# Performance work log

Hardware: AMD Instinct MI355X
Metric: run time of the kernel (lower is better)

## Reference

```python
import jax, jax.numpy as jnp
import numpy as np

B, N, D = 32, 2048, 256


def setup_inputs() -> dict:
    key = jax.random.key(0)
    ks = jax.random.split(key, 9)
    s = 1.0 / np.sqrt(D)
    return {
        "x": jax.random.normal(ks[0], (B, N, D), dtype=jnp.float32),
        "Wq": jax.random.normal(ks[1], (D, D), dtype=jnp.float32) * s,
        "bq": jax.random.normal(ks[2], (D,), dtype=jnp.float32) * s,
        "Wk": jax.random.normal(ks[3], (D, D), dtype=jnp.float32) * s,
        "bk": jax.random.normal(ks[4], (D,), dtype=jnp.float32) * s,
        "Wv": jax.random.normal(ks[5], (D, D), dtype=jnp.float32) * s,
        "bv": jax.random.normal(ks[6], (D,), dtype=jnp.float32) * s,
        "Ww": jax.random.normal(ks[7], (D, 1), dtype=jnp.float32) * s,
        "bw": jax.random.normal(ks[8], (1,), dtype=jnp.float32) * s,
    }


def reference(x, Wq, bq, Wk, bk, Wv, bv, Ww, bw):
    # x: [B, N, D]
    q = jnp.einsum("bnd,de->bne", x, Wq) + bq
    k = jnp.einsum("bnd,de->bne", x, Wk) + bk
    v = jnp.einsum("bnd,de->bne", x, Wv) + bv
    scale = 1.0 / jnp.sqrt(jnp.asarray(q.shape[-1], dtype=q.dtype))
    beta = jnp.einsum("bnd,bmd->bnm", q, k) * scale  # [B, N, N]
    beta = jax.nn.softmax(beta, axis=-1)
    # value.unsqueeze(1) * beta.unsqueeze(-1) summed over dim=2 == beta @ v
    ctx = jnp.einsum("bnm,bmd->bnd", beta, v)  # [B, N, D]
    final_scores = (jnp.einsum("bnd,do->bno", ctx, Ww) + bw).squeeze(-1)  # [B, N]
    return final_scores
```

## Files before the change

kernel.cpp:

```cpp
#include <hip/hip_runtime.h>
#include <hip/hip_fp16.h>

typedef _Float16 half8 __attribute__((ext_vector_type(8)));
typedef float f32x4 __attribute__((ext_vector_type(4)));

#define BB 32
#define NN 2048
#define DD 256
#define QSCALE 0.0625f

__device__ __forceinline__ void gload_lds16(const void* g, void* l) {
    __builtin_amdgcn_global_load_lds(
        (const __attribute__((address_space(1))) void*)g,
        (__attribute__((address_space(3))) void*)l, 16, 0, 0);
}

__global__ void k_pre(const float* __restrict__ Wq, const float* __restrict__ Wk,
                      const float* __restrict__ Wv, const float* __restrict__ bv,
                      const float* __restrict__ Ww, const float* __restrict__ bw,
                      _Float16* __restrict__ Wt, float* __restrict__ wv) {
    if (blockIdx.x < 512) {
        int idx = blockIdx.x * 256 + threadIdx.x;
        int mat = idx >> 16;
        int r = (idx >> 8) & 255;
        int c = idx & 255;
        const float* W = mat ? Wk : Wq;
        Wt[mat * 65536 + c * 256 + r] = (_Float16)W[r * 256 + c];
    } else {
        int gw = ((blockIdx.x - 512) * 256 + (int)threadIdx.x) >> 6;
        int lane = threadIdx.x & 63;
        if (gw > 256) return;
        const float* row = (gw < 256) ? (Wv + gw * 256) : bv;
        f32x4 a = *((const f32x4*)row + lane);
        f32x4 wk = *((const f32x4*)Ww + lane);
        float p = a[0] * wk[0] + a[1] * wk[1] + a[2] * wk[2] + a[3] * wk[3];
        #pragma unroll
        for (int m = 1; m < 64; m <<= 1) p += __shfl_xor(p, m, 64);
        if (lane == 0) wv[gw] = (gw < 256) ? p : (p + bw[0]);
    }
}

__global__ __launch_bounds__(512, 2) void k_proj(
    const float* __restrict__ x, const _Float16* __restrict__ Wt,
    const float* __restrict__ bq, const float* __restrict__ bk,
    const float* __restrict__ wv,
    _Float16* __restrict__ Qh, _Float16* __restrict__ Kh, float* __restrict__ S) {
    __shared__ _Float16 As[128][40];
    int m0 = blockIdx.x * 128;
    int tid = threadIdx.x, w = tid >> 6, l = tid & 63;
    int wr = w >> 2, wc = w & 3;
    int srow = tid >> 2, sc8 = (tid & 3) * 8;
    int lr = l & 15, lg = l >> 4;
    int acol = lg * 8;
    float sacc = 0.f;

    f32x4 zz = {0.f, 0.f, 0.f, 0.f};
    f32x4 acc[2][4][4];
    #pragma unroll
    for (int m = 0; m < 2; ++m)
        #pragma unroll
        for (int i = 0; i < 4; ++i)
            #pragma unroll
            for (int j = 0; j < 4; ++j) acc[m][i][j] = zz;

    for (int k0 = 0; k0 < DD; k0 += 32) {
        __syncthreads();
        {
            const float* src = x + (long)(m0 + srow) * DD + k0 + sc8;
            f32x4 a = *(const f32x4*)src;
            f32x4 b = *(const f32x4*)(src + 4);
            f32x4 wa = *(const f32x4*)(wv + k0 + sc8);
            f32x4 wb = *(const f32x4*)(wv + k0 + sc8 + 4);
            sacc += a[0] * wa[0] + a[1] * wa[1] + a[2] * wa[2] + a[3] * wa[3]
                  + b[0] * wb[0] + b[1] * wb[1] + b[2] * wb[2] + b[3] * wb[3];
            half8 h;
            h[0] = (_Float16)a[0]; h[1] = (_Float16)a[1];
            h[2] = (_Float16)a[2]; h[3] = (_Float16)a[3];
            h[4] = (_Float16)b[0]; h[5] = (_Float16)b[1];
            h[6] = (_Float16)b[2]; h[7] = (_Float16)b[3];
            *(half8*)&As[srow][sc8] = h;
        }
        __syncthreads();
        half8 af[4];
        #pragma unroll
        for (int rt = 0; rt < 4; ++rt)
            af[rt] = *(const half8*)&As[wr * 64 + rt * 16 + lr][acol];
        #pragma unroll
        for (int mat = 0; mat < 2; ++mat)
            #pragma unroll
            for (int ct = 0; ct < 4; ++ct) {
                half8 bf = *(const half8*)(Wt + mat * 65536 +
                                           (long)(wc * 64 + ct * 16 + lr) * DD + k0 + acol);
                #pragma unroll
                for (int rt = 0; rt < 4; ++rt)
                    acc[mat][rt][ct] =
                        __builtin_amdgcn_mfma_f32_16x16x32_f16(af[rt], bf, acc[mat][rt][ct], 0, 0, 0);
            }
    }
    sacc += __shfl_xor(sacc, 1, 64);
    sacc += __shfl_xor(sacc, 2, 64);
    if ((tid & 3) == 0) S[m0 + srow] = sacc + wv[DD];

    #pragma unroll
    for (int mat = 0; mat < 2; ++mat) {
        const float* bias = mat ? bk : bq;
        _Float16* Out = mat ? Kh : Qh;
        float osc = mat ? 1.0f : QSCALE;
        #pragma unroll
        for (int ct = 0; ct < 4; ++ct) {
            int col = wc * 64 + ct * 16 + lr;
            float bi = bias[col];
            #pragma unroll
            for (int rt = 0; rt < 4; ++rt)
                #pragma unroll
                for (int r = 0; r < 4; ++r) {
                    int row = m0 + wr * 64 + rt * 16 + lg * 4 + r;
                    Out[(long)row * DD + col] = (_Float16)((acc[mat][rt][ct][r] + bi) * osc);
                }
        }
    }
}

__global__ __launch_bounds__(512, 2) void k_flash(
    const _Float16* __restrict__ Qh, const _Float16* __restrict__ Kh,
    const float* __restrict__ S, float* __restrict__ out) {
    __shared__ _Float16 Ks[2][2][64][256];
    __shared__ float Ss[2048];
    __shared__ float zred[4][64][8];
    int u = blockIdx.x;
    int b = (u & 7) | (((u >> 3) & 3) << 3);
    int q0 = (u >> 5) * 256;
    const _Float16* Qb = Qh + (long)b * NN * DD;
    const _Float16* Kb = Kh + (long)b * NN * DD;
    const float* Sb = S + b * NN;
    int tid = threadIdx.x, w = tid >> 6, l = tid & 63;
    int lr = l & 15, lg = l >> 4;
    int l5 = l >> 5, c32 = l & 31;
    int qb = w & 3, grp = w >> 2;
    int mbase = grp * 1024;

    half8 qf[4][8];
    #pragma unroll
    for (int qa = 0; qa < 4; ++qa)
        #pragma unroll
        for (int kk = 0; kk < 8; ++kk)
            qf[qa][kk] = *(const half8*)(Qb + (long)(q0 + qb * 64 + qa * 16 + lr) * DD + kk * 32 + lg * 8);

    gload_lds16(Sb + tid * 4, &Ss[(tid & ~63) * 4]);

    #pragma unroll
    for (int i = 0; i < 8; ++i) {
        int r0 = qb * 16 + i * 2;
        int r = r0 + l5;
        gload_lds16(Kb + (long)(mbase + r) * DD + ((c32 ^ (r & 7)) * 8), &Ks[0][grp][r0][0]);
    }
    asm volatile("s_waitcnt vmcnt(0)" ::: "memory");
    __syncthreads();

    float z[4] = {0.f, 0.f, 0.f, 0.f}, y[4] = {0.f, 0.f, 0.f, 0.f};
    int cur = 0;
    for (int t = 0; t < 16; ++t) {
        if (t < 15) {
            #pragma unroll
            for (int i = 0; i < 8; ++i) {
                int r0 = qb * 16 + i * 2;
                int r = r0 + l5;
                gload_lds16(Kb + (long)(mbase + (t + 1) * 64 + r) * DD + ((c32 ^ (r & 7)) * 8),
                            &Ks[cur ^ 1][grp][r0][0]);
            }
        }
        #pragma unroll
        for (int ct = 0; ct < 4; ++ct) {
            f32x4 zz = {0.f, 0.f, 0.f, 0.f};
            f32x4 a[4] = {zz, zz, zz, zz};
            #pragma unroll
            for (int kk = 0; kk < 8; ++kk) {
                half8 kf = *(const half8*)&Ks[cur][grp][ct * 16 + lr][((kk * 4 + lg) ^ (lr & 7)) * 8];
                #pragma unroll
                for (int qa = 0; qa < 4; ++qa)
                    a[qa] = __builtin_amdgcn_mfma_f32_16x16x32_f16(kf, qf[qa][kk], a[qa], 0, 0, 0);
            }
            f32x4 sv = *(const f32x4*)&Ss[mbase + t * 64 + ct * 16 + lg * 4];
            #pragma unroll
            for (int qa = 0; qa < 4; ++qa)
                #pragma unroll
                for (int r = 0; r < 4; ++r) {
                    float e = __expf(a[qa][r]);
                    z[qa] += e;
                    y[qa] = fmaf(e, sv[r], y[qa]);
                }
        }
        asm volatile("s_waitcnt vmcnt(0)" ::: "memory");
        __syncthreads();
        cur ^= 1;
    }
    if (grp == 1) {
        #pragma unroll
        for (int qa = 0; qa < 4; ++qa) {
            zred[qb][l][qa] = z[qa];
            zred[qb][l][qa + 4] = y[qa];
        }
    }
    __syncthreads();
    if (grp == 0) {
        #pragma unroll
        for (int qa = 0; qa < 4; ++qa) {
            z[qa] += zred[qb][l][qa];
            y[qa] += zred[qb][l][qa + 4];
            y[qa] += __shfl_xor(y[qa], 16, 64);
            y[qa] += __shfl_xor(y[qa], 32, 64);
            z[qa] += __shfl_xor(z[qa], 16, 64);
            z[qa] += __shfl_xor(z[qa], 32, 64);
        }
        if (l < 16)
            #pragma unroll
            for (int qa = 0; qa < 4; ++qa)
                out[b * NN + q0 + qb * 64 + qa * 16 + lr] = y[qa] / z[qa];
    }
}

extern "C" void kernel_launch(void* const* d_in, const int* in_sizes, int n_in,
                              void* d_out, int out_size, void* d_ws, size_t ws_size,
                              hipStream_t stream) {
    const float* x  = (const float*)d_in[0];
    const float* Wq = (const float*)d_in[1];
    const float* bq = (const float*)d_in[2];
    const float* Wk = (const float*)d_in[3];
    const float* bk = (const float*)d_in[4];
    const float* Wv = (const float*)d_in[5];
    const float* bv = (const float*)d_in[6];
    const float* Ww = (const float*)d_in[7];
    const float* bw = (const float*)d_in[8];
    char* ws = (char*)d_ws;
    _Float16* Qh = (_Float16*)(ws);
    _Float16* Kh = (_Float16*)(ws + 33554432);
    _Float16* Wt = (_Float16*)(ws + 67108864);
    float* S     = (float*)(ws + 67108864 + 262144);
    float* wv    = (float*)(ws + 67108864 + 262144 + 262144);
    float* outp  = (float*)d_out;

    k_pre<<<dim3(577), dim3(256), 0, stream>>>(Wq, Wk, Wv, bv, Ww, bw, Wt, wv);
    k_proj<<<dim3(512), dim3(512), 0, stream>>>(x, Wt, bq, bk, wv, Qh, Kh, S);
    k_flash<<<dim3(256), dim3(512), 0, stream>>>(Qh, Kh, S, outp);
}
```

Measured before the change: 225.4 us.

## Use 1024-thread flash blocks with exp2 softmax and MFMA priority hints

Doubles the flash kernel's block to 16 waves, each handling 32 query rows instead of 64. This halves per-wave Q register fragments and accumulators so more waves can hide LDS and exp latency. The Q scale is folded with log2(e) so the softmax can use a native exp2 instead of expf, and s_setprio raises priority around the MFMA loop. Risks are higher register pressure under the 1024-thread launch bound and a larger reduction buffer; the K tile load is split across more waves.

```diff
diff --git a/kernel.cpp b/kernel.cpp
--- a/kernel.cpp
+++ b/kernel.cpp
@@ -7,7 +7,7 @@
 #define BB 32
 #define NN 2048
 #define DD 256
-#define QSCALE 0.0625f
+#define QS2 0.09016994374947424f
 
 __device__ __forceinline__ void gload_lds16(const void* g, void* l) {
     __builtin_amdgcn_global_load_lds(
@@ -105,7 +105,7 @@
     for (int mat = 0; mat < 2; ++mat) {
         const float* bias = mat ? bk : bq;
         _Float16* Out = mat ? Kh : Qh;
-        float osc = mat ? 1.0f : QSCALE;
+        float osc = mat ? 1.0f : QS2;
         #pragma unroll
         for (int ct = 0; ct < 4; ++ct) {
             int col = wc * 64 + ct * 16 + lr;
@@ -121,12 +121,12 @@
     }
 }
 
-__global__ __launch_bounds__(512, 2) void k_flash(
+__global__ __launch_bounds__(1024, 4) void k_flash(
     const _Float16* __restrict__ Qh, const _Float16* __restrict__ Kh,
     const float* __restrict__ S, float* __restrict__ out) {
     __shared__ _Float16 Ks[2][2][64][256];
     __shared__ float Ss[2048];
-    __shared__ float zred[4][64][8];
+    __shared__ float zred[8][64][8];
     int u = blockIdx.x;
     int b = (u & 7) | (((u >> 3) & 3) << 3);
     int q0 = (u >> 5) * 256;
@@ -136,34 +136,34 @@
     int tid = threadIdx.x, w = tid >> 6, l = tid & 63;
     int lr = l & 15, lg = l >> 4;
     int l5 = l >> 5, c32 = l & 31;
-    int qb = w & 3, grp = w >> 2;
+    int qs = w & 7, grp = w >> 3;
     int mbase = grp * 1024;
 
-    half8 qf[4][8];
-    #pragma unroll
-    for (int qa = 0; qa < 4; ++qa)
+    half8 qf[2][8];
+    #pragma unroll
+    for (int qa = 0; qa < 2; ++qa)
         #pragma unroll
         for (int kk = 0; kk < 8; ++kk)
-            qf[qa][kk] = *(const half8*)(Qb + (long)(q0 + qb * 64 + qa * 16 + lr) * DD + kk * 32 + lg * 8);
-
-    gload_lds16(Sb + tid * 4, &Ss[(tid & ~63) * 4]);
-
-    #pragma unroll
-    for (int i = 0; i < 8; ++i) {
-        int r0 = qb * 16 + i * 2;
+            qf[qa][kk] = *(const half8*)(Qb + (long)(q0 + qs * 32 + qa * 16 + lr) * DD + kk * 32 + lg * 8);
+
+    if (w < 8) gload_lds16(Sb + tid * 4, &Ss[(tid & ~63) * 4]);
+
+    #pragma unroll
+    for (int i = 0; i < 4; ++i) {
+        int r0 = qs * 8 + i * 2;
         int r = r0 + l5;
         gload_lds16(Kb + (long)(mbase + r) * DD + ((c32 ^ (r & 7)) * 8), &Ks[0][grp][r0][0]);
     }
     asm volatile("s_waitcnt vmcnt(0)" ::: "memory");
     __syncthreads();
 
-    float z[4] = {0.f, 0.f, 0.f, 0.f}, y[4] = {0.f, 0.f, 0.f, 0.f};
+    float z[2] = {0.f, 0.f}, y[2] = {0.f, 0.f};
     int cur = 0;
     for (int t = 0; t < 16; ++t) {
         if (t < 15) {
             #pragma unroll
-            for (int i = 0; i < 8; ++i) {
-                int r0 = qb * 16 + i * 2;
+            for (int i = 0; i < 4; ++i) {
+                int r0 = qs * 8 + i * 2;
                 int r = r0 + l5;
                 gload_lds16(Kb + (long)(mbase + (t + 1) * 64 + r) * DD + ((c32 ^ (r & 7)) * 8),
                             &Ks[cur ^ 1][grp][r0][0]);
@@ -172,20 +172,22 @@
         #pragma unroll
         for (int ct = 0; ct < 4; ++ct) {
             f32x4 zz = {0.f, 0.f, 0.f, 0.f};
-            f32x4 a[4] = {zz, zz, zz, zz};
+            f32x4 a[2] = {zz, zz};
+            __builtin_amdgcn_s_setprio(1);
             #pragma unroll
             for (int kk = 0; kk < 8; ++kk) {
                 half8 kf = *(const half8*)&Ks[cur][grp][ct * 16 + lr][((kk * 4 + lg) ^ (lr & 7)) * 8];
                 #pragma unroll
-                for (int qa = 0; qa < 4; ++qa)
+                for (int qa = 0; qa < 2; ++qa)
                     a[qa] = __builtin_amdgcn_mfma_f32_16x16x32_f16(kf, qf[qa][kk], a[qa], 0, 0, 0);
             }
+            __builtin_amdgcn_s_setprio(0);
             f32x4 sv = *(const f32x4*)&Ss[mbase + t * 64 + ct * 16 + lg * 4];
             #pragma unroll
-            for (int qa = 0; qa < 4; ++qa)
+            for (int qa = 0; qa < 2; ++qa)
                 #pragma unroll
                 for (int r = 0; r < 4; ++r) {
-                    float e = __expf(a[qa][r]);
+                    float e = __builtin_exp2f(a[qa][r]);
                     z[qa] += e;
                     y[qa] = fmaf(e, sv[r], y[qa]);
                 }
@@ -196,17 +198,17 @@
     }
     if (grp == 1) {
         #pragma unroll
-        for (int qa = 0; qa < 4; ++qa) {
-            zred[qb][l][qa] = z[qa];
-            zred[qb][l][qa + 4] = y[qa];
+        for (int qa = 0; qa < 2; ++qa) {
+            zred[qs][l][qa] = z[qa];
+            zred[qs][l][qa + 4] = y[qa];
         }
     }
     __syncthreads();
     if (grp == 0) {
         #pragma unroll
-        for (int qa = 0; qa < 4; ++qa) {
-            z[qa] += zred[qb][l][qa];
-            y[qa] += zred[qb][l][qa + 4];
+        for (int qa = 0; qa < 2; ++qa) {
+            z[qa] += zred[qs][l][qa];
+            y[qa] += zred[qs][l][qa + 4];
             y[qa] += __shfl_xor(y[qa], 16, 64);
             y[qa] += __shfl_xor(y[qa], 32, 64);
             z[qa] += __shfl_xor(z[qa], 16, 64);
@@ -214,8 +216,8 @@
         }
         if (l < 16)
             #pragma unroll
-            for (int qa = 0; qa < 4; ++qa)
-                out[b * NN + q0 + qb * 64 + qa * 16 + lr] = y[qa] / z[qa];
+            for (int qa = 0; qa < 2; ++qa)
+                out[b * NN + q0 + qs * 32 + qa * 16 + lr] = y[qa] / z[qa];
     }
 }
 
@@ -241,5 +243,5 @@
 
     k_pre<<<dim3(577), dim3(256), 0, stream>>>(Wq, Wk, Wv, bv, Ww, bw, Wt, wv);
     k_proj<<<dim3(512), dim3(512), 0, stream>>>(x, Wt, bq, bk, wv, Qh, Kh, S);
-    k_flash<<<dim3(256), dim3(512), 0, stream>>>(Qh, Kh, S, outp);
-}
+    k_flash<<<dim3(256), dim3(1024), 0, stream>>>(Qh, Kh, S, outp);
+}
```

New measurement: 248.4 us. +10.2%, slower.
